# Kernel tuning notes

Measured on AMD Instinct MI355X. Metric: run time of the kernel, lower is better.

Reference implementation:

```python
import jax, jax.numpy as jnp
import numpy as np

# Paged/ragged causal prefill attention (FlashInfer wrapper.run semantics),
# modeled as equal-length batched causal GQA attention.
B, S = 2, 2048          # batch, seq_len (T = B*S tokens, flattened)
H, HKV, D = 32, 8, 128  # query heads, kv heads, head dim
G = H // HKV            # GQA group size
SCALE = 0.08838834764831845  # 1/sqrt(D)


def setup_inputs() -> dict:
    key = jax.random.key(0)
    kq, kk, kv = jax.random.split(key, 3)
    q = jax.random.normal(kq, (B * S, H * D), dtype=jnp.float32)
    k = jax.random.normal(kk, (B * S, HKV * D), dtype=jnp.float32)
    v = jax.random.normal(kv, (B * S, HKV * D), dtype=jnp.float32)
    return {"q": q, "k": k, "v": v}


def reference(q, k, v):
    # q: [T, H*D] -> [B, S, HKV, G, D]; k, v: [T, HKV*D] -> [B, S, HKV, D]
    qh = q.reshape(B, S, HKV, G, D)
    kh = k.reshape(B, S, HKV, D)
    vh = v.reshape(B, S, HKV, D)
    # GQA attention scores: [B, HKV, G, Sq, Sk]
    scores = jnp.einsum('bqhgd,bkhd->bhgqk', qh, kh) * SCALE
    causal = jnp.tril(jnp.ones((S, S), dtype=bool))  # query attends to keys <= its position
    scores = jnp.where(causal, scores, jnp.finfo(scores.dtype).min)
    probs = jax.nn.softmax(scores, axis=-1)
    out = jnp.einsum('bhgqk,bkhd->bqhgd', probs, vh)
    # back to flattened token layout [T, H*D]
    return out.reshape(B * S, H * D)
```

## Files before the change

kernel.cpp:

```cpp
#include <hip/hip_runtime.h>


#define B_   2
#define S_   2048
#define H_   32
#define HKV_ 8
#define D_   128
#define SCALEF 0.08838834764831845f
#define COEF  (SCALEF * 1.44269504088896340736f)
#define DEFER_THR 8.0f

typedef float          f32x4 __attribute__((ext_vector_type(4)));
typedef __bf16         bf16x4 __attribute__((ext_vector_type(4)));
typedef __bf16         bf16x8 __attribute__((ext_vector_type(8)));
typedef unsigned short u16x8 __attribute__((ext_vector_type(8)));

#define MFMA16(a, b, c) __builtin_amdgcn_mfma_f32_16x16x32_bf16((a), (b), (c), 0, 0, 0)

#if defined(__has_builtin)
#if __has_builtin(__builtin_amdgcn_exp2f)
#define EXP2F(x) __builtin_amdgcn_exp2f(x)
#endif
#endif
#ifndef EXP2F
#define EXP2F(x) exp2f(x)
#endif

static __device__ __forceinline__ unsigned short f2bf(float f) {
  unsigned int u = __builtin_bit_cast(unsigned int, f);
  u = (u + 0x7fffu + ((u >> 16) & 1u)) >> 16;
  return (unsigned short)u;
}

static __device__ __forceinline__ void load_lds16(const void* g, void* l) {
  __builtin_amdgcn_global_load_lds(
      (const __attribute__((address_space(1))) void*)g,
      (__attribute__((address_space(3))) void*)l, 16, 0, 0);
}

static __device__ __forceinline__ float swz_x16(float v) {
  return __builtin_bit_cast(
      float, __builtin_amdgcn_ds_swizzle(__builtin_bit_cast(int, v), 0x401F));
}
static __device__ __forceinline__ float bperm_f(int byteaddr, float v) {
  return __builtin_bit_cast(
      float,
      __builtin_amdgcn_ds_bpermute(byteaddr, __builtin_bit_cast(int, v)));
}

__global__ __launch_bounds__(256) void k_convert_kernel(
    const float* __restrict__ k, unsigned short* __restrict__ kbf) {
  int t = blockIdx.x * 256 + threadIdx.x;
  int o = t * 8;
  int d = o & (D_ - 1);
  int s = (o >> 7) & (S_ - 1);
  int bh = o >> 18;
  int b = bh >> 3, hkv = bh & 7;
  const float* src = k + (size_t)(b * S_ + s) * (HKV_ * D_) + hkv * D_ + d;
  f32x4 x0 = *(const f32x4*)src;
  f32x4 x1 = *(const f32x4*)(src + 4);
  u16x8 w;
  w[0] = f2bf(x0[0]); w[1] = f2bf(x0[1]); w[2] = f2bf(x0[2]); w[3] = f2bf(x0[3]);
  w[4] = f2bf(x1[0]); w[5] = f2bf(x1[1]); w[6] = f2bf(x1[2]); w[7] = f2bf(x1[3]);
  *(u16x8*)(kbf + o) = w;
}

__global__ __launch_bounds__(256) void vt_transpose_kernel(
    const float* __restrict__ v, unsigned short* __restrict__ vt) {
  __shared__ float tile[32][65];
  const int tid = threadIdx.x;
  const int s0 = blockIdx.x * 64;
  const int d0 = blockIdx.y * 32;
  const int bh = blockIdx.z;
  const float* src = v + (size_t)(bh >> 3) * S_ * (HKV_ * D_) + (bh & 7) * D_;
#pragma unroll
  for (int it = 0; it < 8; ++it) {
    int idx = it * 256 + tid;
    int sl = idx >> 5, dl = idx & 31;
    tile[dl][sl] = src[(size_t)(s0 + sl) * (HKV_ * D_) + d0 + dl];
  }
  __syncthreads();
  unsigned int* dst = (unsigned int*)vt;
#pragma unroll
  for (int it = 0; it < 4; ++it) {
    int idx = it * 256 + tid;
    int dl = idx >> 5, sp = idx & 31;
    unsigned int w = (unsigned int)f2bf(tile[dl][2 * sp]) |
                     ((unsigned int)f2bf(tile[dl][2 * sp + 1]) << 16);
    dst[(((size_t)bh * D_ + d0 + dl) * S_ + s0 + 2 * sp) >> 1] = w;
  }
}

#define PSTR 72

__global__ __launch_bounds__(256, 2) void attn_kernel(
    const float* __restrict__ qg, const unsigned short* __restrict__ kbfg,
    const unsigned short* __restrict__ vtg, float* __restrict__ outg) {
  __shared__ unsigned short KL[2][2][32 * 128];
  __shared__ unsigned short VL[2][2][128 * 32];
  __shared__ unsigned short PL[4][16 * PSTR];

  const int tid = threadIdx.x;
  const int wave = tid >> 6, lane = tid & 63;
  const int l15 = lane & 15, quad = lane >> 4;
  const int a32 = ((lane ^ 32) << 2);
  const int rowa = quad << 4;

  const int id = (int)blockIdx.x + 16 * (int)blockIdx.y;
  const int xcd = id & 7, slot = id >> 3;
  const int bhkv = xcd * 2 + (slot >> 6);
  const int inner = slot & 63;
  const int g = inner >> 4;
  const int xb = inner & 15;
  const int b = bhkv >> 3, hkv = bhkv & 7;
  const int h = hkv * 4 + g;

  const unsigned short* kbf = kbfg + (size_t)(b * HKV_ + hkv) * S_ * D_;
  const unsigned short* vtb = vtg + (size_t)(b * HKV_ + hkv) * D_ * S_;

  const f32x4 zero4 = {0.f, 0.f, 0.f, 0.f};
  const float NEG_INF = -__builtin_huge_valf();

  auto stage = [&](int kt, int buf) {
#pragma unroll
    for (int sub = 0; sub < 2; ++sub)
#pragma unroll
      for (int j = 0; j < 2; ++j) {
        int si = wave * 128 + j * 64 + lane;
        int kr = si >> 4, pc = si & 15;
        int lc = pc ^ (kr & 15);
        load_lds16(kbf + (size_t)(kt * 64 + sub * 32 + kr) * D_ + lc * 8,
                   &KL[buf][sub][(wave * 128 + j * 64) * 8]);
      }
#pragma unroll
    for (int sub = 0; sub < 2; ++sub)
#pragma unroll
      for (int j = 0; j < 2; ++j) {
        int si = wave * 128 + j * 64 + lane;
        int dr = si >> 2, pc = si & 3;
        int lc = pc ^ ((dr >> 1) & 3);
        load_lds16(vtb + (size_t)dr * S_ + kt * 64 + sub * 32 + lc * 8,
                   &VL[buf][sub][(wave * 128 + j * 64) * 8]);
      }
  };

  for (int ph = 0; ph < 2; ++ph) {
    const int qb = ph ? (31 - xb) : xb;
    const int qbase = qb * 64 + wave * 16;
    const int qgp = qbase + l15;

    bf16x8 qf[4];
#pragma unroll
    for (int ch = 0; ch < 4; ++ch) {
      const float* p = qg + (size_t)(b * S_ + qbase + l15) * (H_ * D_) +
                       h * D_ + ch * 32 + quad * 8;
      f32x4 x0 = *(const f32x4*)p;
      f32x4 x1 = *(const f32x4*)(p + 4);
      bf16x8 t;
      t[0] = (__bf16)(x0[0] * COEF); t[1] = (__bf16)(x0[1] * COEF);
      t[2] = (__bf16)(x0[2] * COEF); t[3] = (__bf16)(x0[3] * COEF);
      t[4] = (__bf16)(x1[0] * COEF); t[5] = (__bf16)(x1[1] * COEF);
      t[6] = (__bf16)(x1[2] * COEF); t[7] = (__bf16)(x1[3] * COEF);
      qf[ch] = t;
    }

    f32x4 acc[8];
#pragma unroll
    for (int dt = 0; dt < 8; ++dt) acc[dt] = zero4;
    float mrow = NEG_INF;
    float lsum = 0.f;

    const int nkt = qb + 1;

    stage(0, 0);
    __syncthreads();

    for (int kt = 0; kt < nkt; ++kt) {
      const int cur = kt & 1;
      if (kt + 1 < nkt) stage(kt + 1, cur ^ 1);

      if (kt * 64 <= qbase + 15) {
        f32x4 sc[4] = {zero4, zero4, zero4, zero4};
#pragma unroll
        for (int h2 = 0; h2 < 4; ++h2) {
          const unsigned short* KS =
              &KL[cur][h2 >> 1][((h2 & 1) * 16 + l15) * D_];
#pragma unroll
          for (int ch = 0; ch < 4; ++ch) {
            const int pc = (ch * 4 + quad) ^ l15;
            u16x8 kf = *(const u16x8*)&KS[pc * 8];
            sc[h2] = MFMA16(__builtin_bit_cast(bf16x8, kf), qf[ch], sc[h2]);
          }
        }
        const int kb0 = kt * 64;
#pragma unroll
        for (int h2 = 0; h2 < 4; ++h2) {
          if (kb0 + h2 * 16 + 15 > qbase) {
            int kb2 = kb0 + h2 * 16 + quad * 4;
#pragma unroll
            for (int r = 0; r < 4; ++r) {
              if (kb2 + r > qgp) sc[h2][r] = NEG_INF;
            }
          }
        }
        float l8 = NEG_INF;
#pragma unroll
        for (int h2 = 0; h2 < 4; ++h2)
          l8 = fmaxf(l8, fmaxf(fmaxf(sc[h2][0], sc[h2][1]),
                               fmaxf(sc[h2][2], sc[h2][3])));
        if (!__all(l8 <= mrow + DEFER_THR)) {
          float t = fmaxf(l8, swz_x16(l8));
          t = fmaxf(t, bperm_f(a32, t));
          float mn = fmaxf(mrow, t);
          float al = EXP2F(mrow - mn);
          mrow = mn;
          lsum *= al;
          f32x4 av;
#pragma unroll
          for (int r = 0; r < 4; ++r) av[r] = bperm_f(rowa + (r << 2), al);
#pragma unroll
          for (int dt = 0; dt < 8; ++dt)
#pragma unroll
            for (int r = 0; r < 4; ++r) acc[dt][r] *= av[r];
        }
#pragma unroll
        for (int h2 = 0; h2 < 4; ++h2)
#pragma unroll
          for (int r = 0; r < 4; ++r) sc[h2][r] = EXP2F(sc[h2][r] - mrow);
#pragma unroll
        for (int h2 = 0; h2 < 4; ++h2)
          lsum += (sc[h2][0] + sc[h2][1]) + (sc[h2][2] + sc[h2][3]);
#pragma unroll
        for (int h2 = 0; h2 < 4; ++h2) {
          bf16x4 w;
          w[0] = (__bf16)sc[h2][0]; w[1] = (__bf16)sc[h2][1];
          w[2] = (__bf16)sc[h2][2]; w[3] = (__bf16)sc[h2][3];
          *(bf16x4*)&PL[wave][l15 * PSTR + h2 * 16 + quad * 4] = w;
        }
#pragma unroll
        for (int kh = 0; kh < 2; ++kh) {
          u16x8 pf = *(const u16x8*)&PL[wave][l15 * PSTR + kh * 32 + quad * 8];
          bf16x8 pb = __builtin_bit_cast(bf16x8, pf);
          const int vsw = (quad ^ ((l15 >> 1) & 3)) * 8;
#pragma unroll
          for (int dt = 0; dt < 8; ++dt) {
            u16x8 vf =
                *(const u16x8*)&VL[cur][kh][(dt * 16 + l15) * 32 + vsw];
            acc[dt] = MFMA16(pb, __builtin_bit_cast(bf16x8, vf), acc[dt]);
          }
        }
      }
      __syncthreads();
    }

    float s = lsum;
    s += swz_x16(s);
    s += bperm_f(a32, s);
    float linv = 1.0f / s;
    f32x4 inv;
#pragma unroll
    for (int r = 0; r < 4; ++r) inv[r] = bperm_f(rowa + (r << 2), linv);
#pragma unroll
    for (int dt = 0; dt < 8; ++dt)
#pragma unroll
      for (int r = 0; r < 4; ++r)
        outg[(size_t)(b * S_ + qbase + quad * 4 + r) * (H_ * D_) +
             h * D_ + dt * 16 + l15] = acc[dt][r] * inv[r];
  }
}

extern "C" void kernel_launch(void* const* d_in, const int* in_sizes, int n_in,
                              void* d_out, int out_size, void* d_ws,
                              size_t ws_size, hipStream_t stream) {
  const float* q = (const float*)d_in[0];
  const float* k = (const float*)d_in[1];
  const float* v = (const float*)d_in[2];
  float* out = (float*)d_out;
  unsigned short* kws = (unsigned short*)d_ws;
  unsigned short* vtws = kws + (size_t)B_ * HKV_ * S_ * D_;

  k_convert_kernel<<<(B_ * S_ * HKV_ * D_ / 8) / 256, 256, 0, stream>>>(k, kws);

  dim3 g1(S_ / 64, D_ / 32, B_ * HKV_);
  vt_transpose_kernel<<<g1, 256, 0, stream>>>(v, vtws);

  dim3 g2(16, B_ * H_);
  attn_kernel<<<g2, 256, 0, stream>>>(q, kws, vtws, out);
}
```

Measured before the change: 240.3 us.

## Triple-buffer 32-key tiles with one barrier, merge prep kernels, raise occupancy

The attention loop now stages 32-key K/V tiles into a three-deep LDS ring. Each iteration waits with an explicit vmcnt and a single s_barrier instead of a trailing __syncthreads, and it uses s_setprio around the MFMA blocks. The smaller tiles and halved P scratch reduce LDS use, which allows three blocks per CU. The K conversion and V transpose kernels are merged into one launch to save launch overhead. The trade-offs are twice as many loop iterations with their softmax and rescale overhead, and reliance on hand-counted vmcnt correctness.

```diff
diff --git a/kernel.cpp b/kernel.cpp
--- a/kernel.cpp
+++ b/kernel.cpp
@@ -48,56 +48,58 @@
       __builtin_amdgcn_ds_bpermute(byteaddr, __builtin_bit_cast(int, v)));
 }
 
-__global__ __launch_bounds__(256) void k_convert_kernel(
-    const float* __restrict__ k, unsigned short* __restrict__ kbf) {
-  int t = blockIdx.x * 256 + threadIdx.x;
-  int o = t * 8;
-  int d = o & (D_ - 1);
-  int s = (o >> 7) & (S_ - 1);
-  int bh = o >> 18;
-  int b = bh >> 3, hkv = bh & 7;
-  const float* src = k + (size_t)(b * S_ + s) * (HKV_ * D_) + hkv * D_ + d;
-  f32x4 x0 = *(const f32x4*)src;
-  f32x4 x1 = *(const f32x4*)(src + 4);
-  u16x8 w;
-  w[0] = f2bf(x0[0]); w[1] = f2bf(x0[1]); w[2] = f2bf(x0[2]); w[3] = f2bf(x0[3]);
-  w[4] = f2bf(x1[0]); w[5] = f2bf(x1[1]); w[6] = f2bf(x1[2]); w[7] = f2bf(x1[3]);
-  *(u16x8*)(kbf + o) = w;
-}
-
-__global__ __launch_bounds__(256) void vt_transpose_kernel(
-    const float* __restrict__ v, unsigned short* __restrict__ vt) {
+__global__ __launch_bounds__(256) void prep_kernel(
+    const float* __restrict__ k, const float* __restrict__ v,
+    unsigned short* __restrict__ kbf, unsigned short* __restrict__ vt) {
   __shared__ float tile[32][65];
   const int tid = threadIdx.x;
-  const int s0 = blockIdx.x * 64;
-  const int d0 = blockIdx.y * 32;
-  const int bh = blockIdx.z;
-  const float* src = v + (size_t)(bh >> 3) * S_ * (HKV_ * D_) + (bh & 7) * D_;
-#pragma unroll
-  for (int it = 0; it < 8; ++it) {
-    int idx = it * 256 + tid;
-    int sl = idx >> 5, dl = idx & 31;
-    tile[dl][sl] = src[(size_t)(s0 + sl) * (HKV_ * D_) + d0 + dl];
+  const int gid = (int)blockIdx.x;
+  if (gid < 2048) {
+    int t = gid * 256 + tid;
+    int o = t * 8;
+    int d = o & (D_ - 1);
+    int s = (o >> 7) & (S_ - 1);
+    int bh = o >> 18;
+    int b = bh >> 3, hkv = bh & 7;
+    const float* src = k + (size_t)(b * S_ + s) * (HKV_ * D_) + hkv * D_ + d;
+    f32x4 x0 = *(const f32x4*)src;
+    f32x4 x1 = *(const f32x4*)(src + 4);
+    u16x8 w;
+    w[0] = f2bf(x0[0]); w[1] = f2bf(x0[1]); w[2] = f2bf(x0[2]); w[3] = f2bf(x0[3]);
+    w[4] = f2bf(x1[0]); w[5] = f2bf(x1[1]); w[6] = f2bf(x1[2]); w[7] = f2bf(x1[3]);
+    *(u16x8*)(kbf + o) = w;
+  } else {
+    const int t = gid - 2048;
+    const int s0 = (t & 31) * 64;
+    const int d0 = ((t >> 5) & 3) * 32;
+    const int bh = t >> 7;
+    const float* src = v + (size_t)(bh >> 3) * S_ * (HKV_ * D_) + (bh & 7) * D_;
+#pragma unroll
+    for (int it = 0; it < 8; ++it) {
+      int idx = it * 256 + tid;
+      int sl = idx >> 5, dl = idx & 31;
+      tile[dl][sl] = src[(size_t)(s0 + sl) * (HKV_ * D_) + d0 + dl];
+    }
+    __syncthreads();
+    unsigned int* dst = (unsigned int*)vt;
+#pragma unroll
+    for (int it = 0; it < 4; ++it) {
+      int idx = it * 256 + tid;
+      int dl = idx >> 5, sp = idx & 31;
+      unsigned int w = (unsigned int)f2bf(tile[dl][2 * sp]) |
+                       ((unsigned int)f2bf(tile[dl][2 * sp + 1]) << 16);
+      dst[(((size_t)bh * D_ + d0 + dl) * S_ + s0 + 2 * sp) >> 1] = w;
+    }
   }
-  __syncthreads();
-  unsigned int* dst = (unsigned int*)vt;
-#pragma unroll
-  for (int it = 0; it < 4; ++it) {
-    int idx = it * 256 + tid;
-    int dl = idx >> 5, sp = idx & 31;
-    unsigned int w = (unsigned int)f2bf(tile[dl][2 * sp]) |
-                     ((unsigned int)f2bf(tile[dl][2 * sp + 1]) << 16);
-    dst[(((size_t)bh * D_ + d0 + dl) * S_ + s0 + 2 * sp) >> 1] = w;
-  }
-}
-
-#define PSTR 72
-
-__global__ __launch_bounds__(256, 2) void attn_kernel(
+}
+
+#define PSTR 36
+
+__global__ __launch_bounds__(256, 3) void attn_kernel(
     const float* __restrict__ qg, const unsigned short* __restrict__ kbfg,
     const unsigned short* __restrict__ vtg, float* __restrict__ outg) {
-  __shared__ unsigned short KL[2][2][32 * 128];
-  __shared__ unsigned short VL[2][2][128 * 32];
+  __shared__ unsigned short KL[3][32 * 128];
+  __shared__ unsigned short VL[3][128 * 32];
   __shared__ unsigned short PL[4][16 * PSTR];
 
   const int tid = threadIdx.x;
@@ -123,31 +125,31 @@
 
   auto stage = [&](int kt, int buf) {
 #pragma unroll
-    for (int sub = 0; sub < 2; ++sub)
-#pragma unroll
-      for (int j = 0; j < 2; ++j) {
-        int si = wave * 128 + j * 64 + lane;
-        int kr = si >> 4, pc = si & 15;
-        int lc = pc ^ (kr & 15);
-        load_lds16(kbf + (size_t)(kt * 64 + sub * 32 + kr) * D_ + lc * 8,
-                   &KL[buf][sub][(wave * 128 + j * 64) * 8]);
-      }
-#pragma unroll
-    for (int sub = 0; sub < 2; ++sub)
-#pragma unroll
-      for (int j = 0; j < 2; ++j) {
-        int si = wave * 128 + j * 64 + lane;
-        int dr = si >> 2, pc = si & 3;
-        int lc = pc ^ ((dr >> 1) & 3);
-        load_lds16(vtb + (size_t)dr * S_ + kt * 64 + sub * 32 + lc * 8,
-                   &VL[buf][sub][(wave * 128 + j * 64) * 8]);
-      }
+    for (int j = 0; j < 2; ++j) {
+      int si = wave * 128 + j * 64 + lane;
+      int kr = si >> 4, pc = si & 15;
+      int lc = pc ^ (kr & 15);
+      load_lds16(kbf + (size_t)(kt * 32 + kr) * D_ + lc * 8,
+                 &KL[buf][(wave * 128 + j * 64) * 8]);
+    }
+#pragma unroll
+    for (int j = 0; j < 2; ++j) {
+      int si = wave * 128 + j * 64 + lane;
+      int dr = si >> 2, pc = si & 3;
+      int lc = pc ^ ((dr >> 1) & 3);
+      load_lds16(vtb + (size_t)dr * S_ + kt * 32 + lc * 8,
+                 &VL[buf][(wave * 128 + j * 64) * 8]);
+    }
   };
 
   for (int ph = 0; ph < 2; ++ph) {
     const int qb = ph ? (31 - xb) : xb;
     const int qbase = qb * 64 + wave * 16;
     const int qgp = qbase + l15;
+
+    __syncthreads();
+    stage(0, 0);
+    stage(1, 1);
 
     bf16x8 qf[4];
 #pragma unroll
@@ -170,31 +172,38 @@
     float mrow = NEG_INF;
     float lsum = 0.f;
 
-    const int nkt = qb + 1;
-
-    stage(0, 0);
-    __syncthreads();
-
+    const int nkt = qb * 2 + 2;
+
+    int cur = 0;
     for (int kt = 0; kt < nkt; ++kt) {
-      const int cur = kt & 1;
-      if (kt + 1 < nkt) stage(kt + 1, cur ^ 1);
-
-      if (kt * 64 <= qbase + 15) {
-        f32x4 sc[4] = {zero4, zero4, zero4, zero4};
-#pragma unroll
-        for (int h2 = 0; h2 < 4; ++h2) {
-          const unsigned short* KS =
-              &KL[cur][h2 >> 1][((h2 & 1) * 16 + l15) * D_];
+      if (kt + 1 < nkt) {
+        asm volatile("s_waitcnt vmcnt(4)" ::: "memory");
+      } else {
+        asm volatile("s_waitcnt vmcnt(0)" ::: "memory");
+      }
+      __builtin_amdgcn_s_barrier();
+      __builtin_amdgcn_sched_barrier(0);
+      int nxt = cur + 2;
+      if (nxt >= 3) nxt -= 3;
+      if (kt + 2 < nkt) stage(kt + 2, nxt);
+
+      if (kt * 32 <= qbase + 15) {
+        f32x4 sc[2] = {zero4, zero4};
+        __builtin_amdgcn_s_setprio(1);
+#pragma unroll
+        for (int h2 = 0; h2 < 2; ++h2) {
+          const int row = h2 * 16 + l15;
 #pragma unroll
           for (int ch = 0; ch < 4; ++ch) {
             const int pc = (ch * 4 + quad) ^ l15;
-            u16x8 kf = *(const u16x8*)&KS[pc * 8];
+            u16x8 kf = *(const u16x8*)&KL[cur][row * D_ + pc * 8];
             sc[h2] = MFMA16(__builtin_bit_cast(bf16x8, kf), qf[ch], sc[h2]);
           }
         }
-        const int kb0 = kt * 64;
-#pragma unroll
-        for (int h2 = 0; h2 < 4; ++h2) {
+        __builtin_amdgcn_s_setprio(0);
+        const int kb0 = kt * 32;
+#pragma unroll
+        for (int h2 = 0; h2 < 2; ++h2) {
           if (kb0 + h2 * 16 + 15 > qbase) {
             int kb2 = kb0 + h2 * 16 + quad * 4;
 #pragma unroll
@@ -203,11 +212,10 @@
             }
           }
         }
-        float l8 = NEG_INF;
-#pragma unroll
-        for (int h2 = 0; h2 < 4; ++h2)
-          l8 = fmaxf(l8, fmaxf(fmaxf(sc[h2][0], sc[h2][1]),
-                               fmaxf(sc[h2][2], sc[h2][3])));
+        float l8 = fmaxf(fmaxf(fmaxf(sc[0][0], sc[0][1]),
+                               fmaxf(sc[0][2], sc[0][3])),
+                         fmaxf(fmaxf(sc[1][0], sc[1][1]),
+                               fmaxf(sc[1][2], sc[1][3])));
         if (!__all(l8 <= mrow + DEFER_THR)) {
           float t = fmaxf(l8, swz_x16(l8));
           t = fmaxf(t, bperm_f(a32, t));
@@ -224,33 +232,35 @@
             for (int r = 0; r < 4; ++r) acc[dt][r] *= av[r];
         }
 #pragma unroll
-        for (int h2 = 0; h2 < 4; ++h2)
+        for (int h2 = 0; h2 < 2; ++h2)
 #pragma unroll
           for (int r = 0; r < 4; ++r) sc[h2][r] = EXP2F(sc[h2][r] - mrow);
-#pragma unroll
-        for (int h2 = 0; h2 < 4; ++h2)
-          lsum += (sc[h2][0] + sc[h2][1]) + (sc[h2][2] + sc[h2][3]);
-#pragma unroll
-        for (int h2 = 0; h2 < 4; ++h2) {
-          bf16x4 w;
-          w[0] = (__bf16)sc[h2][0]; w[1] = (__bf16)sc[h2][1];
-          w[2] = (__bf16)sc[h2][2]; w[3] = (__bf16)sc[h2][3];
-          *(bf16x4*)&PL[wave][l15 * PSTR + h2 * 16 + quad * 4] = w;
-        }
-#pragma unroll
-        for (int kh = 0; kh < 2; ++kh) {
-          u16x8 pf = *(const u16x8*)&PL[wave][l15 * PSTR + kh * 32 + quad * 8];
-          bf16x8 pb = __builtin_bit_cast(bf16x8, pf);
+        lsum += ((sc[0][0] + sc[0][1]) + (sc[0][2] + sc[0][3])) +
+                ((sc[1][0] + sc[1][1]) + (sc[1][2] + sc[1][3]));
+        {
+          bf16x4 w0, w1;
+          w0[0] = (__bf16)sc[0][0]; w0[1] = (__bf16)sc[0][1];
+          w0[2] = (__bf16)sc[0][2]; w0[3] = (__bf16)sc[0][3];
+          w1[0] = (__bf16)sc[1][0]; w1[1] = (__bf16)sc[1][1];
+          w1[2] = (__bf16)sc[1][2]; w1[3] = (__bf16)sc[1][3];
+          *(bf16x4*)&PL[wave][l15 * PSTR + quad * 4] = w0;
+          *(bf16x4*)&PL[wave][l15 * PSTR + 16 + quad * 4] = w1;
+        }
+        {
+          bf16x4 p0 = *(const bf16x4*)&PL[wave][l15 * PSTR + quad * 8];
+          bf16x4 p1 = *(const bf16x4*)&PL[wave][l15 * PSTR + quad * 8 + 4];
+          bf16x8 pb = __builtin_shufflevector(p0, p1, 0, 1, 2, 3, 4, 5, 6, 7);
           const int vsw = (quad ^ ((l15 >> 1) & 3)) * 8;
+          __builtin_amdgcn_s_setprio(1);
 #pragma unroll
           for (int dt = 0; dt < 8; ++dt) {
-            u16x8 vf =
-                *(const u16x8*)&VL[cur][kh][(dt * 16 + l15) * 32 + vsw];
+            u16x8 vf = *(const u16x8*)&VL[cur][(dt * 16 + l15) * 32 + vsw];
             acc[dt] = MFMA16(pb, __builtin_bit_cast(bf16x8, vf), acc[dt]);
           }
+          __builtin_amdgcn_s_setprio(0);
         }
       }
-      __syncthreads();
+      cur = (cur == 2) ? 0 : cur + 1;
     }
 
     float s = lsum;
@@ -279,10 +289,7 @@
   unsigned short* kws = (unsigned short*)d_ws;
   unsigned short* vtws = kws + (size_t)B_ * HKV_ * S_ * D_;
 
-  k_convert_kernel<<<(B_ * S_ * HKV_ * D_ / 8) / 256, 256, 0, stream>>>(k, kws);
-
-  dim3 g1(S_ / 64, D_ / 32, B_ * HKV_);
-  vt_transpose_kernel<<<g1, 256, 0, stream>>>(v, vtws);
+  prep_kernel<<<4096, 256, 0, stream>>>(k, v, kws, vtws);
 
   dim3 g2(16, B_ * H_);
   attn_kernel<<<g2, 256, 0, stream>>>(q, kws, vtws, out);
```

New measurement: 254.0 us. 5.7% more time.
